# Optimization experiments

Hardware: AMD Instinct MI355X
Metric: run time of the kernel (lower is better)

The kernel has to match this reference:

```python
import jax, jax.numpy as jnp
import numpy as np

IN_F = 4096
OUT_F = 4096
GROUP = 128  # group_size divides in_features, so groups are contiguous along in dim


def setup_inputs() -> dict:
    key = jax.random.key(0)
    k1, k2, k3 = jax.random.split(key, 3)
    x = jax.random.normal(k1, (4, 2048, IN_F), dtype=jnp.float32)
    # ternary codes in {-1, 0, +1}
    ternary = (jax.random.randint(k2, (OUT_F, IN_F), 0, 3) - 1).astype(jnp.int8)
    n_groups = OUT_F * IN_F // GROUP
    # per-group positive scales (abs-mean init in the original)
    scales = jax.random.uniform(k3, (n_groups,), dtype=jnp.float32, minval=0.01, maxval=0.1)
    return {"x": x, "ternary": ternary, "scales": scales}


def reference(x, ternary, scales):
    # Dequantize: scales are per contiguous group of GROUP weights in the
    # flattened (out*in) layout; since IN_F % GROUP == 0 this is
    # [OUT_F, IN_F//GROUP] groups along the in dimension.
    s = scales.reshape(OUT_F, IN_F // GROUP, 1)                 # [O, G, 1]
    w = (ternary.astype(jnp.float32).reshape(OUT_F, IN_F // GROUP, GROUP) * s)
    w = w.reshape(OUT_F, IN_F)                                   # dense float weight
    # y = x @ W^T  (F.linear with no bias)
    return jnp.einsum("bsi,oi->bso", x, w)
```

## Files before the change

### kernel.cpp

```cpp
#include <hip/hip_runtime.h>


#define IN_F  4096
#define OUT_F 4096
#define MROWS 8192
#define GROUP 128

#define BM 256
#define BN 128
#define BK 64

using bf16x8  = __attribute__((ext_vector_type(8))) __bf16;
using f32x16  = __attribute__((ext_vector_type(16))) float;

#define GLOBAL_AS __attribute__((address_space(1)))
#define LDS_AS    __attribute__((address_space(3)))

__device__ __forceinline__ unsigned short f2bf(float f) {
  unsigned int u = __float_as_uint(f);
  u += 0x7fffu + ((u >> 16) & 1u);
  return (unsigned short)(u >> 16);
}

#define CVT_BLOCKS ((MROWS * IN_F) / 8 / 256)
#define DQ_BLOCKS  ((OUT_F * IN_F) / 8 / 256)

__global__ void prep_kernel(const float* __restrict__ x, unsigned short* __restrict__ xb,
                            const int* __restrict__ t, const float* __restrict__ s,
                            unsigned short* __restrict__ wb) {
  int b = blockIdx.x;
  if (b < CVT_BLOCKS) {
    const int i = (b * 256 + threadIdx.x) * 8;
    const float4 a0 = *(const float4*)(x + i);
    const float4 a1 = *(const float4*)(x + i + 4);
    union { unsigned short u[8]; uint4 v; } o;
    o.u[0] = f2bf(a0.x); o.u[1] = f2bf(a0.y); o.u[2] = f2bf(a0.z); o.u[3] = f2bf(a0.w);
    o.u[4] = f2bf(a1.x); o.u[5] = f2bf(a1.y); o.u[6] = f2bf(a1.z); o.u[7] = f2bf(a1.w);
    *(uint4*)(xb + i) = o.v;
  } else {
    const int i = ((b - CVT_BLOCKS) * 256 + threadIdx.x) * 8;
    const float sc = s[i >> 7];
    const int4 t0 = *(const int4*)(t + i);
    const int4 t1 = *(const int4*)(t + i + 4);
    union { unsigned short u[8]; uint4 v; } o;
    o.u[0] = f2bf((float)t0.x * sc); o.u[1] = f2bf((float)t0.y * sc);
    o.u[2] = f2bf((float)t0.z * sc); o.u[3] = f2bf((float)t0.w * sc);
    o.u[4] = f2bf((float)t1.x * sc); o.u[5] = f2bf((float)t1.y * sc);
    o.u[6] = f2bf((float)t1.z * sc); o.u[7] = f2bf((float)t1.w * sc);
    *(uint4*)(wb + i) = o.v;
  }
}

__global__ __launch_bounds__(256, 2) void gemm_bt_kernel(const unsigned short* __restrict__ A,
                                                         const unsigned short* __restrict__ B,
                                                         float* __restrict__ C) {
  __shared__ unsigned short As[BM * BK];
  __shared__ unsigned short Bs[BN * BK];

  const int tid  = threadIdx.x;
  const int lane = tid & 63;
  const int wv   = tid >> 6;
  const int wm   = wv & 1;
  const int wn   = wv >> 1;
  const int r32  = lane & 31;
  const int half = lane >> 5;

  const int m0 = blockIdx.y * BM;
  const int n0 = blockIdx.x * BN;

  const int srow = lane >> 3;
  const int scol = ((lane & 7) ^ srow) * 8;

  f32x16 acc[4][2];
#pragma unroll
  for (int i = 0; i < 4; ++i)
#pragma unroll
    for (int j = 0; j < 2; ++j)
      acc[i][j] = (f32x16)(0.0f);

  for (int k0 = 0; k0 < IN_F; k0 += BK) {
#pragma unroll
    for (int i = 0; i < 8; ++i) {
      const int chunk = wv * 8 + i;
      const int row   = chunk * 8 + srow;
      const unsigned short* ga = A + (size_t)(m0 + row) * IN_F + (k0 + scol);
      __builtin_amdgcn_global_load_lds((const GLOBAL_AS unsigned int*)ga,
                                       (LDS_AS unsigned int*)(As + chunk * 512),
                                       16, 0, 0);
    }
#pragma unroll
    for (int i = 0; i < 4; ++i) {
      const int chunk = wv * 4 + i;
      const int row   = chunk * 8 + srow;
      const unsigned short* gb = B + (size_t)(n0 + row) * IN_F + (k0 + scol);
      __builtin_amdgcn_global_load_lds((const GLOBAL_AS unsigned int*)gb,
                                       (LDS_AS unsigned int*)(Bs + chunk * 512),
                                       16, 0, 0);
    }
    __syncthreads();

#pragma unroll
    for (int ks = 0; ks < BK; ks += 16) {
      const int pc = (((ks >> 3) + half) ^ (lane & 7)) * 8;
      bf16x8 af[4], bfr[2];
#pragma unroll
      for (int t = 0; t < 4; ++t)
        af[t] = *(const bf16x8*)(As + (wm * 128 + t * 32 + r32) * BK + pc);
#pragma unroll
      for (int t = 0; t < 2; ++t)
        bfr[t] = *(const bf16x8*)(Bs + (wn * 64 + t * 32 + r32) * BK + pc);
#pragma unroll
      for (int i = 0; i < 4; ++i)
#pragma unroll
        for (int j = 0; j < 2; ++j)
          acc[i][j] = __builtin_amdgcn_mfma_f32_32x32x16_bf16(af[i], bfr[j], acc[i][j], 0, 0, 0);
    }
    __syncthreads();
  }

#pragma unroll
  for (int i = 0; i < 4; ++i)
#pragma unroll
    for (int j = 0; j < 2; ++j) {
      const int ncol  = n0 + wn * 64 + j * 32 + r32;
      const int mbase = m0 + wm * 128 + i * 32 + 4 * half;
#pragma unroll
      for (int r = 0; r < 16; ++r) {
        const int mrow = mbase + (r & 3) + 8 * (r >> 2);
        C[(size_t)mrow * OUT_F + ncol] = acc[i][j][r];
      }
    }
}

extern "C" void kernel_launch(void* const* d_in, const int* in_sizes, int n_in,
                              void* d_out, int out_size, void* d_ws, size_t ws_size,
                              hipStream_t stream) {
  const float* x       = (const float*)d_in[0];
  const int*   ternary = (const int*)d_in[1];
  const float* scales  = (const float*)d_in[2];
  float* out = (float*)d_out;

  unsigned short* xb = (unsigned short*)d_ws;
  unsigned short* wb = xb + (size_t)MROWS * IN_F;

  prep_kernel<<<CVT_BLOCKS + DQ_BLOCKS, 256, 0, stream>>>(x, xb, ternary, scales, wb);

  dim3 grid(OUT_F / BN, MROWS / BM);
  gemm_bt_kernel<<<grid, 256, 0, stream>>>(xb, wb, out);
}
```

Measured before the change: 524.0 us.

## Rewrite GEMM as 256x256 double-buffered 8-wave kernel with XCD-aware block mapping

Replaces the 256x128 single-buffered GEMM with a 256x256 tile computed by 512 threads. The kernel uses a 128KB LDS double buffer with fine-grained staged global_load_lds, explicit vmcnt waits and barriers, MFMA priority boosting, and a new swizzle. Block indices are remapped so that blocks on the same XCD share A/B tiles in L2. The prep kernel becomes a grid-stride loop over 2048 blocks. The aim is to hide memory latency behind MFMA work and raise arithmetic intensity, at the cost of fragile hand-tuned synchronization and high LDS use that limits occupancy.

```diff
diff --git a/kernel.cpp b/kernel.cpp
--- a/kernel.cpp
+++ b/kernel.cpp
@@ -7,11 +7,15 @@
 #define GROUP 128
 
 #define BM 256
-#define BN 128
+#define BN 256
 #define BK 64
-
-using bf16x8  = __attribute__((ext_vector_type(8))) __bf16;
-using f32x16  = __attribute__((ext_vector_type(16))) float;
+#define NKT   (IN_F / BK)
+#define NITER (NKT / 2)
+
+#define PREP_BLOCKS 2048
+
+using bf16x8 = __attribute__((ext_vector_type(8))) __bf16;
+using f32x16 = __attribute__((ext_vector_type(16))) float;
 
 #define GLOBAL_AS __attribute__((address_space(1)))
 #define LDS_AS    __attribute__((address_space(3)))
@@ -22,40 +26,44 @@
   return (unsigned short)(u >> 16);
 }
 
-#define CVT_BLOCKS ((MROWS * IN_F) / 8 / 256)
-#define DQ_BLOCKS  ((OUT_F * IN_F) / 8 / 256)
-
 __global__ void prep_kernel(const float* __restrict__ x, unsigned short* __restrict__ xb,
                             const int* __restrict__ t, const float* __restrict__ s,
                             unsigned short* __restrict__ wb) {
-  int b = blockIdx.x;
-  if (b < CVT_BLOCKS) {
-    const int i = (b * 256 + threadIdx.x) * 8;
-    const float4 a0 = *(const float4*)(x + i);
-    const float4 a1 = *(const float4*)(x + i + 4);
+  const int stride = PREP_BLOCKS * 256;
+  const int gid = blockIdx.x * 256 + threadIdx.x;
+  for (int i = gid; i < (MROWS * IN_F) / 8; i += stride) {
+    const int e = i * 8;
+    const float4 a0 = *(const float4*)(x + e);
+    const float4 a1 = *(const float4*)(x + e + 4);
     union { unsigned short u[8]; uint4 v; } o;
     o.u[0] = f2bf(a0.x); o.u[1] = f2bf(a0.y); o.u[2] = f2bf(a0.z); o.u[3] = f2bf(a0.w);
     o.u[4] = f2bf(a1.x); o.u[5] = f2bf(a1.y); o.u[6] = f2bf(a1.z); o.u[7] = f2bf(a1.w);
-    *(uint4*)(xb + i) = o.v;
-  } else {
-    const int i = ((b - CVT_BLOCKS) * 256 + threadIdx.x) * 8;
-    const float sc = s[i >> 7];
-    const int4 t0 = *(const int4*)(t + i);
-    const int4 t1 = *(const int4*)(t + i + 4);
+    *(uint4*)(xb + e) = o.v;
+  }
+  for (int i = gid; i < (OUT_F * IN_F) / 8; i += stride) {
+    const int e = i * 8;
+    const float sc = s[e >> 7];
+    const int4 t0 = *(const int4*)(t + e);
+    const int4 t1 = *(const int4*)(t + e + 4);
     union { unsigned short u[8]; uint4 v; } o;
     o.u[0] = f2bf((float)t0.x * sc); o.u[1] = f2bf((float)t0.y * sc);
     o.u[2] = f2bf((float)t0.z * sc); o.u[3] = f2bf((float)t0.w * sc);
     o.u[4] = f2bf((float)t1.x * sc); o.u[5] = f2bf((float)t1.y * sc);
     o.u[6] = f2bf((float)t1.z * sc); o.u[7] = f2bf((float)t1.w * sc);
-    *(uint4*)(wb + i) = o.v;
-  }
-}
-
-__global__ __launch_bounds__(256, 2) void gemm_bt_kernel(const unsigned short* __restrict__ A,
+    *(uint4*)(wb + e) = o.v;
+  }
+}
+
+
+#define FENCE asm volatile("" ::: "memory")
+#define BAR() do { FENCE; __builtin_amdgcn_s_barrier(); FENCE; } while (0)
+#define VMBAR(N) do { asm volatile("s_waitcnt vmcnt(" #N ")" ::: "memory"); \
+                      __builtin_amdgcn_s_barrier(); FENCE; } while (0)
+
+__global__ __launch_bounds__(512, 2) void gemm_bt_kernel(const unsigned short* __restrict__ A,
                                                          const unsigned short* __restrict__ B,
                                                          float* __restrict__ C) {
-  __shared__ unsigned short As[BM * BK];
-  __shared__ unsigned short Bs[BN * BK];
+  __shared__ unsigned short lds[65536];
 
   const int tid  = threadIdx.x;
   const int lane = tid & 63;
@@ -63,73 +71,151 @@
   const int wm   = wv & 1;
   const int wn   = wv >> 1;
   const int r32  = lane & 31;
-  const int half = lane >> 5;
-
-  const int m0 = blockIdx.y * BM;
-  const int n0 = blockIdx.x * BN;
+  const int kh   = lane >> 5;
+
+  const int bid = blockIdx.x;
+  const int xcd = bid & 7;
+  const int loc = bid >> 3;
+  const int by  = (xcd >> 1) * 8 + (loc >> 3);
+  const int bx  = (xcd & 1) * 8 + (loc & 7);
+  const int m0  = by * BM;
+  const int n0  = bx * BN;
 
   const int srow = lane >> 3;
-  const int scol = ((lane & 7) ^ srow) * 8;
-
-  f32x16 acc[4][2];
-#pragma unroll
-  for (int i = 0; i < 4; ++i)
-#pragma unroll
-    for (int j = 0; j < 2; ++j)
-      acc[i][j] = (f32x16)(0.0f);
-
-  for (int k0 = 0; k0 < IN_F; k0 += BK) {
-#pragma unroll
-    for (int i = 0; i < 8; ++i) {
-      const int chunk = wv * 8 + i;
-      const int row   = chunk * 8 + srow;
-      const unsigned short* ga = A + (size_t)(m0 + row) * IN_F + (k0 + scol);
-      __builtin_amdgcn_global_load_lds((const GLOBAL_AS unsigned int*)ga,
-                                       (LDS_AS unsigned int*)(As + chunk * 512),
-                                       16, 0, 0);
+  const int l7   = lane & 7;
+  const int rowoff0 = (wv * 2 + 0) * 8 + srow;
+  const int rowoff1 = (wv * 2 + 1) * 8 + srow;
+  const int sc0 = (l7 ^ srow ^ ((wv * 2 + 0) & 7)) * 8;
+  const int sc1 = (l7 ^ srow ^ ((wv * 2 + 1) & 7)) * 8;
+  const unsigned short* pA0 = A + (size_t)(m0 + rowoff0) * IN_F + sc0;
+  const unsigned short* pA1 = A + (size_t)(m0 + rowoff1) * IN_F + sc1;
+  const unsigned short* pB0 = B + (size_t)(n0 + rowoff0) * IN_F + sc0;
+  const unsigned short* pB1 = B + (size_t)(n0 + rowoff1) * IN_F + sc1;
+
+#define STAGE_A(bufi, h, kcol) do { \
+    __builtin_amdgcn_global_load_lds((const GLOBAL_AS unsigned int*)(pA0 + (size_t)(h) * 128 * IN_F + (kcol)), \
+        (LDS_AS unsigned int*)((char*)lds + (bufi) * 32768 + (h) * 16384 + (wv * 2 + 0) * 1024), 16, 0, 0); \
+    __builtin_amdgcn_global_load_lds((const GLOBAL_AS unsigned int*)(pA1 + (size_t)(h) * 128 * IN_F + (kcol)), \
+        (LDS_AS unsigned int*)((char*)lds + (bufi) * 32768 + (h) * 16384 + (wv * 2 + 1) * 1024), 16, 0, 0); \
+  } while (0)
+
+#define STAGE_B(bufi, h, kcol) do { \
+    __builtin_amdgcn_global_load_lds((const GLOBAL_AS unsigned int*)(pB0 + (size_t)(h) * 128 * IN_F + (kcol)), \
+        (LDS_AS unsigned int*)((char*)lds + 65536 + (bufi) * 32768 + (h) * 16384 + (wv * 2 + 0) * 1024), 16, 0, 0); \
+    __builtin_amdgcn_global_load_lds((const GLOBAL_AS unsigned int*)(pB1 + (size_t)(h) * 128 * IN_F + (kcol)), \
+        (LDS_AS unsigned int*)((char*)lds + 65536 + (bufi) * 32768 + (h) * 16384 + (wv * 2 + 1) * 1024), 16, 0, 0); \
+  } while (0)
+
+  const int rA = wm * 64 + r32;
+  const int rB = wn * 32 + r32;
+  int offA[2][4];
+  int offB[4];
+#pragma unroll
+  for (int sm = 0; sm < 2; ++sm) {
+    const int fh = ((sm * 4) + (r32 >> 3)) & 7;
+#pragma unroll
+    for (int k4 = 0; k4 < 4; ++k4) {
+      const int pc = (2 * k4 + kh) ^ (r32 & 7) ^ fh;
+      offA[sm][k4] = (rA + sm * 32) * 128 + pc * 16;
     }
-#pragma unroll
-    for (int i = 0; i < 4; ++i) {
-      const int chunk = wv * 4 + i;
-      const int row   = chunk * 8 + srow;
-      const unsigned short* gb = B + (size_t)(n0 + row) * IN_F + (k0 + scol);
-      __builtin_amdgcn_global_load_lds((const GLOBAL_AS unsigned int*)gb,
-                                       (LDS_AS unsigned int*)(Bs + chunk * 512),
-                                       16, 0, 0);
+  }
+  {
+    const int fh = ((wn * 4) + (r32 >> 3)) & 7;
+#pragma unroll
+    for (int k4 = 0; k4 < 4; ++k4) {
+      const int pc = (2 * k4 + kh) ^ (r32 & 7) ^ fh;
+      offB[k4] = 65536 + rB * 128 + pc * 16;
     }
-    __syncthreads();
-
-#pragma unroll
-    for (int ks = 0; ks < BK; ks += 16) {
-      const int pc = (((ks >> 3) + half) ^ (lane & 7)) * 8;
-      bf16x8 af[4], bfr[2];
-#pragma unroll
-      for (int t = 0; t < 4; ++t)
-        af[t] = *(const bf16x8*)(As + (wm * 128 + t * 32 + r32) * BK + pc);
-#pragma unroll
-      for (int t = 0; t < 2; ++t)
-        bfr[t] = *(const bf16x8*)(Bs + (wn * 64 + t * 32 + r32) * BK + pc);
-#pragma unroll
-      for (int i = 0; i < 4; ++i)
-#pragma unroll
-        for (int j = 0; j < 2; ++j)
-          acc[i][j] = __builtin_amdgcn_mfma_f32_32x32x16_bf16(af[i], bfr[j], acc[i][j], 0, 0, 0);
-    }
-    __syncthreads();
-  }
-
-#pragma unroll
-  for (int i = 0; i < 4; ++i)
-#pragma unroll
-    for (int j = 0; j < 2; ++j) {
-      const int ncol  = n0 + wn * 64 + j * 32 + r32;
-      const int mbase = m0 + wm * 128 + i * 32 + 4 * half;
-#pragma unroll
-      for (int r = 0; r < 16; ++r) {
-        const int mrow = mbase + (r & 3) + 8 * (r >> 2);
-        C[(size_t)mrow * OUT_F + ncol] = acc[i][j][r];
+  }
+
+  bf16x8 af[2][4], bf[2][4];
+
+#define READ_A(bufi, qm) do { \
+    _Pragma("unroll") for (int sm = 0; sm < 2; ++sm) \
+    _Pragma("unroll") for (int k4 = 0; k4 < 4; ++k4) \
+      af[sm][k4] = *(const bf16x8*)((const char*)lds + offA[sm][k4] + (bufi) * 32768 + (qm) * 16384); \
+  } while (0)
+
+#define READ_B(bufi, qn) do { \
+    _Pragma("unroll") for (int k4 = 0; k4 < 4; ++k4) \
+      bf[qn][k4] = *(const bf16x8*)((const char*)lds + offB[k4] + (bufi) * 32768 + (qn) * 16384); \
+  } while (0)
+
+#define MFMA_Q(qm, qn) do { \
+    __builtin_amdgcn_s_setprio(1); \
+    _Pragma("unroll") for (int sm = 0; sm < 2; ++sm) \
+    _Pragma("unroll") for (int k4 = 0; k4 < 4; ++k4) \
+      acc[qm][sm][qn] = __builtin_amdgcn_mfma_f32_32x32x16_bf16(af[sm][k4], bf[qn][k4], acc[qm][sm][qn], 0, 0, 0); \
+    __builtin_amdgcn_s_setprio(0); \
+  } while (0)
+
+  f32x16 acc[2][2][2];
+#pragma unroll
+  for (int a = 0; a < 2; ++a)
+#pragma unroll
+    for (int b = 0; b < 2; ++b)
+#pragma unroll
+      for (int c = 0; c < 2; ++c)
+        acc[a][b][c] = (f32x16)(0.0f);
+
+  STAGE_A(0, 0, 0); STAGE_B(0, 0, 0); STAGE_B(0, 1, 0); STAGE_A(0, 1, 0);
+  STAGE_A(1, 0, BK); STAGE_B(1, 0, BK); STAGE_B(1, 1, BK);
+  VMBAR(6);
+
+#pragma unroll 1
+  for (int j = 0; j < NITER; ++j) {
+    const int ku = (2 * j + 1) * BK;
+    const int k2 = (2 * j + 2) * BK;
+    const int k3 = (2 * j + 3) * BK;
+    const bool more = (j < NITER - 1);
+
+    READ_A(0, 0); READ_B(0, 0);
+    STAGE_A(1, 1, ku);
+    BAR(); MFMA_Q(0, 0); BAR();
+
+    READ_B(0, 1);
+    if (more) STAGE_A(0, 0, k2);
+    BAR(); MFMA_Q(0, 1); BAR();
+
+    READ_A(0, 1);
+    if (more) STAGE_B(0, 0, k2);
+    BAR(); MFMA_Q(1, 0); BAR();
+
+    if (more) STAGE_B(0, 1, k2);
+    BAR(); MFMA_Q(1, 1);
+    if (more) { VMBAR(6); } else { VMBAR(0); }
+
+    READ_A(1, 0); READ_B(1, 0);
+    if (more) STAGE_A(0, 1, k2);
+    BAR(); MFMA_Q(0, 0); BAR();
+
+    READ_B(1, 1);
+    if (more) STAGE_A(1, 0, k3);
+    BAR(); MFMA_Q(0, 1); BAR();
+
+    READ_A(1, 1);
+    if (more) STAGE_B(1, 0, k3);
+    BAR(); MFMA_Q(1, 0); BAR();
+
+    if (more) STAGE_B(1, 1, k3);
+    BAR(); MFMA_Q(1, 1);
+    if (more) { VMBAR(6); } else { BAR(); }
+  }
+
+#pragma unroll
+  for (int qm = 0; qm < 2; ++qm)
+#pragma unroll
+    for (int sm = 0; sm < 2; ++sm)
+#pragma unroll
+      for (int qn = 0; qn < 2; ++qn) {
+        const int ncol = n0 + qn * 128 + wn * 32 + r32;
+        const int mb   = m0 + qm * 128 + wm * 64 + sm * 32 + 4 * kh;
+#pragma unroll
+        for (int r = 0; r < 16; ++r) {
+          const int mrow = mb + (r & 3) + 8 * (r >> 2);
+          C[(size_t)mrow * OUT_F + ncol] = acc[qm][sm][qn][r];
+        }
       }
-    }
 }
 
 extern "C" void kernel_launch(void* const* d_in, const int* in_sizes, int n_in,
@@ -143,8 +229,7 @@
   unsigned short* xb = (unsigned short*)d_ws;
   unsigned short* wb = xb + (size_t)MROWS * IN_F;
 
-  prep_kernel<<<CVT_BLOCKS + DQ_BLOCKS, 256, 0, stream>>>(x, xb, ternary, scales, wb);
-
-  dim3 grid(OUT_F / BN, MROWS / BM);
-  gemm_bt_kernel<<<grid, 256, 0, stream>>>(xb, wb, out);
-}
+  prep_kernel<<<PREP_BLOCKS, 256, 0, stream>>>(x, xb, ternary, scales, wb);
+
+  gemm_bt_kernel<<<(MROWS / BM) * (OUT_F / BN), 512, 0, stream>>>(xb, wb, out);
+}
```

Measured after the change: 525.5 us. Within noise of the previous version (+0.3%).
